# Performance work log

Measured on AMD Instinct MI355X. Metric: run time of the kernel, lower is better.

The kernel has to match this reference:

```python
import jax, jax.numpy as jnp
import numpy as np

D_MODEL = 1024
N_HEADS = 16
HEAD_DIM = D_MODEL // N_HEADS
D_FF = 4096
B, S = 2, 2048


def layer_norm(x, gamma, beta, eps=1e-5):
    mu = jnp.mean(x, axis=-1, keepdims=True)
    var = jnp.mean(jnp.square(x - mu), axis=-1, keepdims=True)
    return (x - mu) * jax.lax.rsqrt(var + eps) * gamma + beta


def setup_inputs() -> dict:
    key = jax.random.key(0)
    ks = jax.random.split(key, 8)
    s = 0.02
    return {
        "x": jax.random.normal(ks[0], (B, S, D_MODEL), dtype=jnp.float32),
        "qkv_w": jax.random.normal(ks[1], (D_MODEL, 3 * D_MODEL), dtype=jnp.float32) * s,
        "qkv_b": jnp.zeros((3 * D_MODEL,), jnp.float32),
        "out_w": jax.random.normal(ks[2], (D_MODEL, D_MODEL), dtype=jnp.float32) * s,
        "out_b": jnp.zeros((D_MODEL,), jnp.float32),
        "attn_ln_g": jnp.ones((D_MODEL,), jnp.float32),
        "attn_ln_b": jnp.zeros((D_MODEL,), jnp.float32),
        "norm1_g": jnp.ones((D_MODEL,), jnp.float32),
        "norm1_b": jnp.zeros((D_MODEL,), jnp.float32),
        "ff_ln_g": jnp.ones((D_MODEL,), jnp.float32),
        "ff_ln_b": jnp.zeros((D_MODEL,), jnp.float32),
        "w1": jax.random.normal(ks[3], (D_MODEL, D_FF), dtype=jnp.float32) * s,
        "b1": jnp.zeros((D_FF,), jnp.float32),
        "w2": jax.random.normal(ks[4], (D_FF, D_MODEL), dtype=jnp.float32) * s,
        "b2": jnp.zeros((D_MODEL,), jnp.float32),
        "norm2_g": jnp.ones((D_MODEL,), jnp.float32),
        "norm2_b": jnp.zeros((D_MODEL,), jnp.float32),
    }


def reference(x, qkv_w, qkv_b, out_w, out_b, attn_ln_g, attn_ln_b,
              norm1_g, norm1_b, ff_ln_g, ff_ln_b, w1, b1, w2, b2,
              norm2_g, norm2_b):
    # --- MultiHeadAttention (pre-LN inside the attn block) ---
    h = layer_norm(x, attn_ln_g, attn_ln_b)
    qkv = h @ qkv_w + qkv_b                       # [B,S,3D]
    qkv = qkv.reshape(B, S, 3, N_HEADS, HEAD_DIM)
    q = jnp.transpose(qkv[:, :, 0], (0, 2, 1, 3))  # [B,H,S,hd]
    k = jnp.transpose(qkv[:, :, 1], (0, 2, 1, 3))
    v = jnp.transpose(qkv[:, :, 2], (0, 2, 1, 3))
    scale = HEAD_DIM ** -0.5
    scores = jnp.einsum("bhqd,bhkd->bhqk", q, k) * scale  # [B,H,S,S]
    attn = jax.nn.softmax(scores, axis=-1)
    ctx = jnp.einsum("bhqk,bhkd->bhqd", attn, v)
    ctx = jnp.transpose(ctx, (0, 2, 1, 3)).reshape(B, S, D_MODEL)
    attn_out = ctx @ out_w + out_b

    # residual + post-LN
    x = layer_norm(x + attn_out, norm1_g, norm1_b)

    # --- FeedForward (pre-LN inside the FF block, GELU) ---
    h = layer_norm(x, ff_ln_g, ff_ln_b)
    ff = jax.nn.gelu(h @ w1 + b1, approximate=False) @ w2 + b2

    # residual + post-LN
    return layer_norm(x + ff, norm2_g, norm2_b)
```

## Files before the change

kernel.cpp:

```cpp
#include <hip/hip_runtime.h>
#include <hip/hip_bf16.h>

typedef __attribute__((ext_vector_type(4))) float f32x4;
typedef __attribute__((ext_vector_type(16))) float f32x16;
typedef __attribute__((ext_vector_type(8))) short s16x8;
typedef __attribute__((ext_vector_type(4))) short s16x4;

#define DM 1024
#define NH 16
#define NB 2
#define NS 2048
#define NTOK (NB*NS)

__device__ __forceinline__ float b2f(short u){
  union { unsigned int i; float f; } c; c.i = ((unsigned int)(unsigned short)u) << 16; return c.f;
}
__device__ __forceinline__ short f2b(float f){
  __hip_bfloat16 h = __float2bfloat16(f);
  return __builtin_bit_cast(short, h);
}
__device__ __forceinline__ unsigned pk2(float lo, float hi){
  unsigned ul = __builtin_bit_cast(unsigned, lo);
  unsigned uh = __builtin_bit_cast(unsigned, hi);
  return (uh & 0xFFFF0000u) | (ul >> 16);
}
__device__ __forceinline__ float ex2(float x){
  float r;
  asm("v_exp_f32 %0, %1" : "=v"(r) : "v"(x));
  return r;
}
__device__ __forceinline__ float rcpf(float x){
  float r;
  asm("v_rcp_f32 %0, %1" : "=v"(r) : "v"(x));
  return r;
}
__device__ __forceinline__ void gload16(const void* g, void* l){
  __builtin_amdgcn_global_load_lds((const __attribute__((address_space(1))) void*)g,
                                   (__attribute__((address_space(3))) void*)l, 16, 0, 0);
}
__device__ __forceinline__ s16x4 tr16(const void* p){
  s16x4 r;
  asm volatile("ds_read_b64_tr_b16 %0, %1"
               : "=v"(r)
               : "v"((const __attribute__((address_space(3))) short*)p)
               : "memory");
  return r;
}

#define BARX { __builtin_amdgcn_sched_barrier(0); __builtin_amdgcn_s_barrier(); __builtin_amdgcn_sched_barrier(0); }
#define LGK  { asm volatile("s_waitcnt lgkmcnt(0)" ::: "memory"); __builtin_amdgcn_sched_barrier(0); }

template<int MIH>
__device__ __forceinline__ void rdA(s16x8 (&Af)[4][2], const short* Ab, int foff){
  #pragma unroll
  for (int m=0;m<4;m++)
    #pragma unroll
    for (int ks=0;ks<2;ks++)
      Af[m][ks] = *(const s16x8*)(Ab + (MIH*4+m)*1024 + ks*512 + foff);
}
template<int NIH>
__device__ __forceinline__ void rdB(s16x8 (&Bf)[4][2], const short* Bb, int foff){
  #pragma unroll
  for (int n=0;n<2;n++)
    #pragma unroll
    for (int ks=0;ks<2;ks++)
      Bf[NIH*2+n][ks] = *(const s16x8*)(Bb + (NIH*2+n)*1024 + ks*512 + foff);
}
template<int MIH,int NIH>
__device__ __forceinline__ void mmQ(f32x4 (&acc)[8][4], s16x8 (&Af)[4][2], s16x8 (&Bf)[4][2]){
  __builtin_amdgcn_s_setprio(1);
  #pragma unroll
  for (int m=0;m<4;m++)
    #pragma unroll
    for (int n=0;n<2;n++)
      #pragma unroll
      for (int ks=0;ks<2;ks++)
        acc[MIH*4+m][NIH*2+n] = __builtin_amdgcn_mfma_f32_16x16x32_bf16(
            Af[m][ks], Bf[NIH*2+n][ks], acc[MIH*4+m][NIH*2+n], 0,0,0);
  __builtin_amdgcn_s_setprio(0);
}

template<int GELU, int SPLITS>
__global__ __launch_bounds__(512,2) void gemm8p(
    const short* __restrict__ A, const short* __restrict__ Bt,
    const float* __restrict__ bias,
    short* __restrict__ C0, short* __restrict__ C1,
    short* __restrict__ C2, short* __restrict__ C3,
    int M, int N, int Ktot)
{
  __shared__ short Al[2*16384];
  __shared__ short Bl[2*16384];
  int tid = threadIdx.x, wid = tid>>6, lane = tid&63;
  int la = lane&15, lb = lane>>4;
  int z = blockIdx.z;
  const int Ksp = Ktot / SPLITS;
  short* C = (SPLITS==1) ? C0 : (z==0?C0 : z==1?C1 : z==2?C2 : C3);
  const short* Az  = A  + z*Ksp;
  const short* Btz = Bt + z*Ksp;
  int nbn = N>>8;
  int nwg = (M>>8)*nbn;
  int bid = (int)blockIdx.x;
  int sid = (bid&7)*(nwg>>3) + (bid>>3);
  int bm = sid / nbn, bn = sid % nbn;
  int wm2 = wid>>2, wn4 = wid&3;
  int bhalf = wn4>>1, bq4 = (wn4&1)*4;

  const short* aA0 = Az  + (size_t)(bm*256)*Ktot;
  const short* aA1 = Az  + (size_t)(bm*256+128)*Ktot;
  const short* bB0 = Btz + (size_t)(bn*256)*Ktot;
  const short* bB1 = Btz + (size_t)(bn*256+128)*Ktot;

  auto stG = [&](short* dstHalf, const short* srcRow0, int kt){
    #pragma unroll
    for (int c=0;c<2;c++){
      int s = c*8 + wid;
      int row = ((s>>1)<<4) + (lane>>2);
      int kk  = kt + ((s&1)<<5) + (((lane&3)<<3) ^ ((lane&32)>>1));
      gload16(srcRow0 + (size_t)row*Ktot + kk, dstHalf + s*512);
    }
  };

  int NJ = Ksp>>7;
  stG(&Al[0], aA0, 0);      stG(&Al[8192], aA1, 0);
  stG(&Bl[0], bB0, 0);      stG(&Bl[8192], bB1, 0);
  stG(&Bl[16384], bB0, 64); stG(&Bl[16384+8192], bB1, 64);
  asm volatile("s_waitcnt vmcnt(4)" ::: "memory");
  BARX;

  f32x4 acc[8][4] = {};
  s16x8 Af[4][2], Bf[4][2];
  int foff = la*32 + ((lb*8) ^ ((la&8)<<1));

  const short* Ab0c = &Al[wm2*8192];
  const short* Ab1c = &Al[16384 + wm2*8192];
  const short* Bb0c = &Bl[bhalf*8192 + bq4*1024];
  const short* Bb1c = &Bl[16384 + bhalf*8192 + bq4*1024];

  for (int j=0;j<NJ;j++){
    bool more = (j+1 < NJ);
    int ktA  = (2*j+1)*64;
    int ktN0 = (2*j+2)*64, ktN1 = (2*j+3)*64;
    rdA<0>(Af, Ab0c, foff); rdB<0>(Bf, Bb0c, foff);
    stG(&Al[16384], aA0, ktA);
    BARX; LGK; mmQ<0,0>(acc,Af,Bf); BARX;
    rdB<1>(Bf, Bb0c, foff);
    stG(&Al[16384+8192], aA1, ktA);
    BARX; LGK; mmQ<0,1>(acc,Af,Bf); BARX;
    rdA<1>(Af, Ab0c, foff);
    if (more) stG(&Bl[0], bB0, ktN0);
    BARX; LGK; mmQ<1,1>(acc,Af,Bf); BARX;
    if (more){ stG(&Bl[8192], bB1, ktN0);
               asm volatile("s_waitcnt vmcnt(4)" ::: "memory"); }
    else     { asm volatile("s_waitcnt vmcnt(0)" ::: "memory"); }
    BARX; mmQ<1,0>(acc,Af,Bf); BARX;
    rdA<0>(Af, Ab1c, foff); rdB<0>(Bf, Bb1c, foff);
    if (more) stG(&Al[0], aA0, ktN0);
    BARX; LGK; mmQ<0,0>(acc,Af,Bf); BARX;
    rdB<1>(Bf, Bb1c, foff);
    if (more) stG(&Al[8192], aA1, ktN0);
    BARX; LGK; mmQ<0,1>(acc,Af,Bf); BARX;
    rdA<1>(Af, Ab1c, foff);
    if (more) stG(&Bl[16384], bB0, ktN1);
    BARX; LGK; mmQ<1,1>(acc,Af,Bf); BARX;
    if (more){ stG(&Bl[16384+8192], bB1, ktN1);
               asm volatile("s_waitcnt vmcnt(4)" ::: "memory"); }
    else     { asm volatile("s_waitcnt vmcnt(0)" ::: "memory"); }
    BARX; mmQ<1,0>(acc,Af,Bf); BARX;
  }

  short* halfC = wm2 ? Bl : Al;
  #pragma unroll
  for (int ni=0;ni<4;ni++){
    int col = wn4*64 + ni*16 + la;
    float bv = (SPLITS==1 || z==0) ? bias[bn*256 + col] : 0.0f;
    #pragma unroll
    for (int mi=0;mi<8;mi++){
      int rloc = mi*16 + lb*4;
      #pragma unroll
      for (int j=0;j<4;j++){
        float v = acc[mi][ni][j] + bv;
        if (GELU){
          float xx = v;
          float y = xx*(0.79788456f + 0.035677408f*xx*xx);
          float p = ex2(2.88539008f*y);
          v = xx - xx*rcpf(p + 1.0f);
        }
        halfC[(rloc+j)*256 + col] = f2b(v);
      }
    }
  }
  BARX;
  #pragma unroll
  for (int i=0;i<8;i++){
    int row = i*32 + (tid>>4);
    int colc = (tid&15)*16;
    const short* src = (i<4) ? &Al[(row&127)*256 + colc] : &Bl[(row&127)*256 + colc];
    s16x8 v0 = *(const s16x8*)src;
    s16x8 v1 = *(const s16x8*)(src+8);
    short* dst = &C[(size_t)(bm*256+row)*N + bn*256 + colc];
    *(s16x8*)dst = v0;
    *(s16x8*)(dst+8) = v1;
  }
}

__global__ __launch_bounds__(512,1) void attn_fwd(const short* __restrict__ qkv, short* __restrict__ ctx)
{
  __shared__ short KlS[2*4096];
  __shared__ short VlS[2*4096];
  __shared__ float stats[8*32];
  char* Kl = (char*)KlS; char* Vl = (char*)VlS;
  int tid=threadIdx.x, w=tid>>6, lane=tid&63;
  int q5=lane&31, hi=lane>>5, la=lane&15, lb0=(lane>>4)&1;
  int qt=blockIdx.x, bh=blockIdx.y;
  int b=bh>>4, h=bh&15;
  int q0w = qt*256 + w*32;

  const float QSC = 0.125f * 1.44269504f;
  const short* qp = qkv + (size_t)(b*NS+q0w+q5)*3072 + h*64 + hi*8;
  s16x8 qf[4];
  #pragma unroll
  for (int ds=0; ds<4; ds++){
    s16x8 v = *(const s16x8*)(qp + ds*16);
    #pragma unroll
    for (int j=0;j<8;j++) v[j] = f2b(b2f(v[j])*QSC);
    qf[ds]=v;
  }

  int krow = 8*w + (lane>>3);
  int kcolS = (((lane&7) ^ ((lane>>3)&7)) << 3);
  const short* Ksrc = qkv + (size_t)(b*NS+krow)*3072 + h*64 + 1024 + kcolS;
  int vk = 16*(w&3) + 8*hi + 4*lb0 + ((lane>>1)&3);
  int vd = 32*(w>>2) + 16*((lane>>3)&1) + 8*(lane&1);
  const short* Vsrc = qkv + (size_t)(b*NS+vk)*3072 + h*64 + 2048 + vd;

  int sw = (q5&7)<<4;
  int baseK = q5*128 + ((hi<<4) ^ (sw&16)) + (sw&96);
  int baseV = hi*512 + lb0*128 + la*8;

  f32x16 cacc0={}, cacc1={};
  float mrow=-1e30f, lrow=0.f;
  const size_t tstep = (size_t)64*3072;

  gload16(Ksrc, Kl + w*1024);
  gload16(Vsrc, Vl + w*1024);
  __syncthreads();
  int cur=0;

  for (int t=0;t<NS/64;t++){
    if (t+1 < NS/64){
      gload16(Ksrc + (size_t)(t+1)*tstep, Kl + (cur^1)*8192 + w*1024);
      gload16(Vsrc + (size_t)(t+1)*tstep, Vl + (cur^1)*8192 + w*1024);
    }
    const char* Kb = Kl + cur*8192;
    f32x16 s0={}, s1={};
    #pragma unroll
    for (int ds=0; ds<4; ds++){
      s16x8 k0 = *(const s16x8*)(Kb + (baseK ^ (ds<<5)));
      s16x8 k1 = *(const s16x8*)(Kb + 4096 + (baseK ^ (ds<<5)));
      s0 = __builtin_amdgcn_mfma_f32_32x32x16_bf16(k0, qf[ds], s0, 0,0,0);
      s1 = __builtin_amdgcn_mfma_f32_32x32x16_bf16(k1, qf[ds], s1, 0,0,0);
    }
    float pmax = s0[0];
    #pragma unroll
    for (int r=1;r<16;r++) pmax = fmaxf(pmax, s0[r]);
    #pragma unroll
    for (int r=0;r<16;r++) pmax = fmaxf(pmax, s1[r]);
    pmax = fmaxf(pmax, __shfl_xor(pmax, 32, 64));
    if (__any(pmax > mrow + 8.f)){
      float mnew = fmaxf(mrow, pmax);
      float corr = ex2(mrow - mnew);
      if (!hi) stats[w*32+q5] = corr;
      LGK;
      lrow *= corr; mrow = mnew;
      #pragma unroll
      for (int r=0;r<16;r++){
        float c = stats[w*32 + ((r&3)+8*(r>>2)+4*hi)];
        cacc0[r]*=c; cacc1[r]*=c;
      }
    }
    float rs = 0.f;
    #pragma unroll
    for (int r=0;r<16;r++){ float p=ex2(s0[r]-mrow); s0[r]=p; rs+=p; }
    #pragma unroll
    for (int r=0;r<16;r++){ float p=ex2(s1[r]-mrow); s1[r]=p; rs+=p; }
    rs += __shfl_xor(rs, 32, 64);
    lrow += rs;
    unsigned int D0[4][2], D1[4][2], R0[4][2], R1[4][2];
    #pragma unroll
    for (int bb=0;bb<4;bb++)
      #pragma unroll
      for (int hh=0;hh<2;hh++){
        D0[bb][hh] = pk2(s0[4*bb+2*hh], s0[4*bb+2*hh+1]);
        D1[bb][hh] = pk2(s1[4*bb+2*hh], s1[4*bb+2*hh+1]);
      }
    #pragma unroll
    for (int bb=0;bb<4;bb++)
      #pragma unroll
      for (int hh=0;hh<2;hh++){
        R0[bb][hh] = (unsigned int)__shfl_xor((int)D0[bb][hh], 32, 64);
        R1[bb][hh] = (unsigned int)__shfl_xor((int)D1[bb][hh], 32, 64);
      }
    union PA { unsigned int u[4]; s16x8 v; } pa[4];
    #pragma unroll
    for (int e=0;e<2;e++)
      #pragma unroll
      for (int hh=0;hh<2;hh++){
        pa[e].u[hh]     = hi ? R0[2*e+1][hh] : D0[2*e][hh];
        pa[e].u[2+hh]   = hi ? D0[2*e+1][hh] : R0[2*e][hh];
        pa[2+e].u[hh]   = hi ? R1[2*e+1][hh] : D1[2*e][hh];
        pa[2+e].u[2+hh] = hi ? D1[2*e+1][hh] : R1[2*e][hh];
      }
    const char* Vb = Vl + cur*8192;
    #pragma unroll
    for (int ks=0;ks<4;ks++){
      s16x4 t00 = tr16(Vb + ks*1024 +        0 + baseV);
      s16x4 t01 = tr16(Vb + ks*1024 +      256 + baseV);
      s16x4 t10 = tr16(Vb + ks*1024 + 4096     + baseV);
      s16x4 t11 = tr16(Vb + ks*1024 + 4096+256 + baseV);
      LGK;
      union { s16x4 hh[2]; s16x8 v; } u0, u1;
      u0.hh[0]=t00; u0.hh[1]=t01;
      u1.hh[0]=t10; u1.hh[1]=t11;
      cacc0 = __builtin_amdgcn_mfma_f32_32x32x16_bf16(pa[ks].v, u0.v, cacc0, 0,0,0);
      cacc1 = __builtin_amdgcn_mfma_f32_32x32x16_bf16(pa[ks].v, u1.v, cacc1, 0,0,0);
    }
    __syncthreads();
    cur ^= 1;
  }
  if (!hi) stats[w*32+q5] = 1.0f/lrow;
  LGK;
  #pragma unroll
  for (int r=0;r<16;r++){
    int q = (r&3)+8*(r>>2)+4*hi;
    float linv = stats[w*32+q];
    size_t row = (size_t)(b*NS + q0w + q)*DM + h*64;
    ctx[row + q5]      = f2b(cacc0[r]*linv);
    ctx[row + 32 + q5] = f2b(cacc1[r]*linv);
  }
}

__device__ __forceinline__ void wred2(float& s, float& ss){
  #pragma unroll
  for (int m=1;m<64;m<<=1){ s += __shfl_xor(s,m,64); ss += __shfl_xor(ss,m,64); }
}

__global__ __launch_bounds__(256) void ln_in(const float* __restrict__ x,
    const float* __restrict__ g, const float* __restrict__ be, short* __restrict__ out)
{
  int row=blockIdx.x, tid=threadIdx.x;
  __shared__ float r1[4], r2[4];
  float4 v = ((const float4*)(x + (size_t)row*DM))[tid];
  float s=v.x+v.y+v.z+v.w, ss=v.x*v.x+v.y*v.y+v.z*v.z+v.w*v.w;
  wred2(s,ss);
  if ((tid&63)==0){ r1[tid>>6]=s; r2[tid>>6]=ss; }
  __syncthreads();
  s=r1[0]+r1[1]+r1[2]+r1[3]; ss=r2[0]+r2[1]+r2[2]+r2[3];
  float mu=s*(1.f/DM);
  float rstd=rsqrtf(ss*(1.f/DM)-mu*mu+1e-5f);
  float4 gv=((const float4*)g)[tid], bv=((const float4*)be)[tid];
  s16x4 o;
  o[0]=f2b((v.x-mu)*rstd*gv.x+bv.x);
  o[1]=f2b((v.y-mu)*rstd*gv.y+bv.y);
  o[2]=f2b((v.z-mu)*rstd*gv.z+bv.z);
  o[3]=f2b((v.w-mu)*rstd*gv.w+bv.w);
  *(s16x4*)(out + (size_t)row*DM + tid*4) = o;
}

__global__ __launch_bounds__(256) void ln_chain(const float* __restrict__ x,
    const short* __restrict__ p0, const short* __restrict__ p1,
    const short* __restrict__ p2, const short* __restrict__ p3,
    const float* __restrict__ g1, const float* __restrict__ be1,
    const float* __restrict__ g2, const float* __restrict__ be2,
    float* __restrict__ x1, short* __restrict__ h2)
{
  int row=blockIdx.x, tid=threadIdx.x;
  __shared__ float r1[4], r2[4], r3[4], r4[4];
  size_t off = (size_t)row*DM + tid*4;
  float4 xv = ((const float4*)(x + (size_t)row*DM))[tid];
  s16x4 a0=*(const s16x4*)(p0+off), a1=*(const s16x4*)(p1+off);
  s16x4 a2=*(const s16x4*)(p2+off), a3=*(const s16x4*)(p3+off);
  float4 y;
  y.x = xv.x + b2f(a0[0])+b2f(a1[0])+b2f(a2[0])+b2f(a3[0]);
  y.y = xv.y + b2f(a0[1])+b2f(a1[1])+b2f(a2[1])+b2f(a3[1]);
  y.z = xv.z + b2f(a0[2])+b2f(a1[2])+b2f(a2[2])+b2f(a3[2]);
  y.w = xv.w + b2f(a0[3])+b2f(a1[3])+b2f(a2[3])+b2f(a3[3]);
  float s=y.x+y.y+y.z+y.w, ss=y.x*y.x+y.y*y.y+y.z*y.z+y.w*y.w;
  wred2(s,ss);
  if ((tid&63)==0){ r1[tid>>6]=s; r2[tid>>6]=ss; }
  __syncthreads();
  s=r1[0]+r1[1]+r1[2]+r1[3]; ss=r2[0]+r2[1]+r2[2]+r2[3];
  float mu=s*(1.f/DM);
  float rstd=rsqrtf(ss*(1.f/DM)-mu*mu+1e-5f);
  float4 g1v=((const float4*)g1)[tid], b1v=((const float4*)be1)[tid];
  float4 xo;
  xo.x=(y.x-mu)*rstd*g1v.x+b1v.x;
  xo.y=(y.y-mu)*rstd*g1v.y+b1v.y;
  xo.z=(y.z-mu)*rstd*g1v.z+b1v.z;
  xo.w=(y.w-mu)*rstd*g1v.w+b1v.w;
  ((float4*)(x1 + (size_t)row*DM))[tid] = xo;
  float s2=xo.x+xo.y+xo.z+xo.w, ss2=xo.x*xo.x+xo.y*xo.y+xo.z*xo.z+xo.w*xo.w;
  wred2(s2,ss2);
  if ((tid&63)==0){ r3[tid>>6]=s2; r4[tid>>6]=ss2; }
  __syncthreads();
  s2=r3[0]+r3[1]+r3[2]+r3[3]; ss2=r4[0]+r4[1]+r4[2]+r4[3];
  float mu2=s2*(1.f/DM);
  float rstd2=rsqrtf(ss2*(1.f/DM)-mu2*mu2+1e-5f);
  float4 g2v=((const float4*)g2)[tid], b2v=((const float4*)be2)[tid];
  s16x4 o;
  o[0]=f2b((xo.x-mu2)*rstd2*g2v.x+b2v.x);
  o[1]=f2b((xo.y-mu2)*rstd2*g2v.y+b2v.y);
  o[2]=f2b((xo.z-mu2)*rstd2*g2v.z+b2v.z);
  o[3]=f2b((xo.w-mu2)*rstd2*g2v.w+b2v.w);
  *(s16x4*)(h2 + off) = o;
}

__global__ __launch_bounds__(256) void ln_out_k(const float* __restrict__ x1,
    const short* __restrict__ p0, const short* __restrict__ p1,
    const short* __restrict__ p2, const short* __restrict__ p3,
    const float* __restrict__ g, const float* __restrict__ be, float* __restrict__ out)
{
  int row=blockIdx.x, tid=threadIdx.x;
  __shared__ float r1[4], r2[4];
  size_t off = (size_t)row*DM + tid*4;
  float4 xv = ((const float4*)(x1 + (size_t)row*DM))[tid];
  s16x4 a0=*(const s16x4*)(p0+off), a1=*(const s16x4*)(p1+off);
  s16x4 a2=*(const s16x4*)(p2+off), a3=*(const s16x4*)(p3+off);
  float4 y;
  y.x = xv.x + b2f(a0[0])+b2f(a1[0])+b2f(a2[0])+b2f(a3[0]);
  y.y = xv.y + b2f(a0[1])+b2f(a1[1])+b2f(a2[1])+b2f(a3[1]);
  y.z = xv.z + b2f(a0[2])+b2f(a1[2])+b2f(a2[2])+b2f(a3[2]);
  y.w = xv.w + b2f(a0[3])+b2f(a1[3])+b2f(a2[3])+b2f(a3[3]);
  float s=y.x+y.y+y.z+y.w, ss=y.x*y.x+y.y*y.y+y.z*y.z+y.w*y.w;
  wred2(s,ss);
  if ((tid&63)==0){ r1[tid>>6]=s; r2[tid>>6]=ss; }
  __syncthreads();
  s=r1[0]+r1[1]+r1[2]+r1[3]; ss=r2[0]+r2[1]+r2[2]+r2[3];
  float mu=s*(1.f/DM);
  float rstd=rsqrtf(ss*(1.f/DM)-mu*mu+1e-5f);
  float4 gv=((const float4*)g)[tid], bv=((const float4*)be)[tid];
  float4 o;
  o.x=(y.x-mu)*rstd*gv.x+bv.x;
  o.y=(y.y-mu)*rstd*gv.y+bv.y;
  o.z=(y.z-mu)*rstd*gv.z+bv.z;
  o.w=(y.w-mu)*rstd*gv.w+bv.w;
  ((float4*)(out + (size_t)row*DM))[tid] = o;
}

__global__ __launch_bounds__(256) void cast_t(const float* __restrict__ w, short* __restrict__ wt, int R, int C)
{
  __shared__ short t[64][65];
  int nbr = R>>6;
  int br = (int)blockIdx.x % nbr, bc = (int)blockIdx.x / nbr;
  int tid = threadIdx.x;
  #pragma unroll
  for (int i=0;i<4;i++){
    int c = i*256 + tid;
    int r = c>>4, c4 = (c&15)*4;
    float4 v = *(const float4*)(w + (size_t)(br*64 + r)*C + bc*64 + c4);
    t[r][c4+0]=f2b(v.x); t[r][c4+1]=f2b(v.y); t[r][c4+2]=f2b(v.z); t[r][c4+3]=f2b(v.w);
  }
  __syncthreads();
  #pragma unroll
  for (int i=0;i<4;i++){
    int c = i*256 + tid;
    int oc = c>>4, c4 = (c&15)*4;
    s16x4 p;
    p[0]=t[c4+0][oc]; p[1]=t[c4+1][oc]; p[2]=t[c4+2][oc]; p[3]=t[c4+3][oc];
    *(s16x4*)&wt[(size_t)(bc*64 + oc)*R + br*64 + c4] = p;
  }
}

extern "C" void kernel_launch(void* const* d_in, const int* in_sizes, int n_in,
                              void* d_out, int out_size, void* d_ws, size_t ws_size,
                              hipStream_t stream)
{
  const float* x      = (const float*)d_in[0];
  const float* qkv_w  = (const float*)d_in[1];
  const float* qkv_b  = (const float*)d_in[2];
  const float* out_w  = (const float*)d_in[3];
  const float* out_b  = (const float*)d_in[4];
  const float* aln_g  = (const float*)d_in[5];
  const float* aln_b  = (const float*)d_in[6];
  const float* n1_g   = (const float*)d_in[7];
  const float* n1_b   = (const float*)d_in[8];
  const float* fln_g  = (const float*)d_in[9];
  const float* fln_b  = (const float*)d_in[10];
  const float* w1     = (const float*)d_in[11];
  const float* b1     = (const float*)d_in[12];
  const float* w2     = (const float*)d_in[13];
  const float* b2     = (const float*)d_in[14];
  const float* n2_g   = (const float*)d_in[15];
  const float* n2_b   = (const float*)d_in[16];

  char* ws = (char*)d_ws;
  short* w2T   = (short*)(ws + 0);
  short* w1T   = (short*)(ws + 8388608);
  short* woutT = (short*)(ws + 16777216);
  short* wqkvT = (short*)(ws + 18874368);
  short* h1    = (short*)(ws + 25165824);
  short* qkv   = (short*)(ws + 33554432);
  short* ctx   = (short*)(ws + 58720256);
  float* x1    = (float*)(ws + 67108864);
  short* ff1   = (short*)(ws + 33554432);
  short* Po0 = (short*)(ws + 25165824);
  short* Po1 = (short*)(ws + 33554432);
  short* Po2 = (short*)(ws + 41943040);
  short* Po3 = (short*)(ws + 50331648);
  short* Pf0 = (short*)(ws + 8388608);
  short* Pf1 = (short*)(ws + 16777216);
  short* Pf2 = (short*)(ws + 25165824);
  short* Pf3 = (short*)(ws + 83886080);
  float* outp  = (float*)d_out;

  cast_t<<<dim3(16*48),256,0,stream>>>(qkv_w, wqkvT, 1024, 3072);
  cast_t<<<dim3(16*16),256,0,stream>>>(out_w, woutT, 1024, 1024);
  cast_t<<<dim3(16*64),256,0,stream>>>(w1,    w1T,   1024, 4096);
  cast_t<<<dim3(64*16),256,0,stream>>>(w2,    w2T,   4096, 1024);

  ln_in<<<NTOK,256,0,stream>>>(x, aln_g, aln_b, h1);
  gemm8p<0,1><<<dim3(192,1,1),512,0,stream>>>(h1, wqkvT, qkv_b, qkv,qkv,qkv,qkv, 4096,3072,1024);
  attn_fwd<<<dim3(8,32),512,0,stream>>>(qkv, ctx);
  gemm8p<0,4><<<dim3(64,1,4),512,0,stream>>>(ctx, woutT, out_b, Po0,Po1,Po2,Po3, 4096,1024,1024);
  ln_chain<<<NTOK,256,0,stream>>>(x, Po0,Po1,Po2,Po3, n1_g,n1_b, fln_g,fln_b, x1, h1);
  gemm8p<1,1><<<dim3(256,1,1),512,0,stream>>>(h1, w1T, b1, ff1,ff1,ff1,ff1, 4096,4096,1024);
  gemm8p<0,4><<<dim3(64,1,4),512,0,stream>>>(ff1, w2T, b2, Pf0,Pf1,Pf2,Pf3, 4096,1024,4096);
  ln_out_k<<<NTOK,256,0,stream>>>(x1, Pf0,Pf1,Pf2,Pf3, n2_g,n2_b, outp);
}
```

Before: 260.3 us.

## Split attention over the key dimension into two halves and merge partial results

Attention now runs split-K (flash-decoding style): each block handles half of the key sequence, grid z=2, and writes a normalized partial output plus per-row max and sum. A new merge kernel combines the two partials with log-sum-exp weights into ctx. This doubles the block count from 256 to 512 so the 256-CU GPU is filled better, and launch bounds allow 2 blocks per CU. The cost is an extra kernel launch, extra bf16 partial traffic, a second rounding to bf16, and workspace buffer reshuffling that must avoid aliasing.

```diff
diff --git a/kernel.cpp b/kernel.cpp
--- a/kernel.cpp
+++ b/kernel.cpp
@@ -203,7 +203,8 @@
   }
 }
 
-__global__ __launch_bounds__(512,1) void attn_fwd(const short* __restrict__ qkv, short* __restrict__ ctx)
+__global__ __launch_bounds__(512,2) void attn_fwd(const short* __restrict__ qkv,
+    short* __restrict__ Op0, short* __restrict__ Op1, float* __restrict__ ml)
 {
   __shared__ short KlS[2*4096];
   __shared__ short VlS[2*4096];
@@ -211,9 +212,12 @@
   char* Kl = (char*)KlS; char* Vl = (char*)VlS;
   int tid=threadIdx.x, w=tid>>6, lane=tid&63;
   int q5=lane&31, hi=lane>>5, la=lane&15, lb0=(lane>>4)&1;
-  int qt=blockIdx.x, bh=blockIdx.y;
+  int qt=blockIdx.x, bh=blockIdx.y, z=blockIdx.z;
   int b=bh>>4, h=bh&15;
   int q0w = qt*256 + w*32;
+  short* Od = z ? Op1 : Op0;
+  float* Md = ml + z*131072;
+  float* Ld = Md + 65536;
 
   const float QSC = 0.125f * 1.44269504f;
   const short* qp = qkv + (size_t)(b*NS+q0w+q5)*3072 + h*64 + hi*8;
@@ -226,12 +230,13 @@
     qf[ds]=v;
   }
 
+  const size_t tstep = (size_t)64*3072;
   int krow = 8*w + (lane>>3);
   int kcolS = (((lane&7) ^ ((lane>>3)&7)) << 3);
-  const short* Ksrc = qkv + (size_t)(b*NS+krow)*3072 + h*64 + 1024 + kcolS;
+  const short* Ksrc = qkv + (size_t)(b*NS+krow)*3072 + h*64 + 1024 + kcolS + (size_t)(z*16)*tstep;
   int vk = 16*(w&3) + 8*hi + 4*lb0 + ((lane>>1)&3);
   int vd = 32*(w>>2) + 16*((lane>>3)&1) + 8*(lane&1);
-  const short* Vsrc = qkv + (size_t)(b*NS+vk)*3072 + h*64 + 2048 + vd;
+  const short* Vsrc = qkv + (size_t)(b*NS+vk)*3072 + h*64 + 2048 + vd + (size_t)(z*16)*tstep;
 
   int sw = (q5&7)<<4;
   int baseK = q5*128 + ((hi<<4) ^ (sw&16)) + (sw&96);
@@ -239,15 +244,14 @@
 
   f32x16 cacc0={}, cacc1={};
   float mrow=-1e30f, lrow=0.f;
-  const size_t tstep = (size_t)64*3072;
 
   gload16(Ksrc, Kl + w*1024);
   gload16(Vsrc, Vl + w*1024);
   __syncthreads();
   int cur=0;
 
-  for (int t=0;t<NS/64;t++){
-    if (t+1 < NS/64){
+  for (int t=0;t<16;t++){
+    if (t+1 < 16){
       gload16(Ksrc + (size_t)(t+1)*tstep, Kl + (cur^1)*8192 + w*1024);
       gload16(Vsrc + (size_t)(t+1)*tstep, Vl + (cur^1)*8192 + w*1024);
     }
@@ -327,16 +331,43 @@
     __syncthreads();
     cur ^= 1;
   }
-  if (!hi) stats[w*32+q5] = 1.0f/lrow;
+  if (!hi){
+    stats[w*32+q5] = 1.0f/lrow;
+    Md[bh*2048 + q0w + q5] = mrow;
+    Ld[bh*2048 + q0w + q5] = lrow;
+  }
   LGK;
   #pragma unroll
   for (int r=0;r<16;r++){
     int q = (r&3)+8*(r>>2)+4*hi;
     float linv = stats[w*32+q];
     size_t row = (size_t)(b*NS + q0w + q)*DM + h*64;
-    ctx[row + q5]      = f2b(cacc0[r]*linv);
-    ctx[row + 32 + q5] = f2b(cacc1[r]*linv);
-  }
+    Od[row + q5]      = f2b(cacc0[r]*linv);
+    Od[row + 32 + q5] = f2b(cacc1[r]*linv);
+  }
+}
+
+__global__ __launch_bounds__(256) void attn_mrg(const short* __restrict__ O0,
+    const short* __restrict__ O1, const float* __restrict__ ml, short* __restrict__ ctx)
+{
+  int r = blockIdx.x, tid = threadIdx.x;
+  int b = r>>11, q = r&2047;
+  int c = tid*4;
+  int h = c>>6;
+  int idx = (b*16+h)*2048 + q;
+  float m0 = ml[idx],        l0 = ml[65536+idx];
+  float m1 = ml[131072+idx], l1 = ml[196608+idx];
+  float M = fmaxf(m0,m1);
+  float w0 = l0*ex2(m0-M), w1 = l1*ex2(m1-M);
+  float inv = rcpf(w0+w1);
+  w0 *= inv; w1 *= inv;
+  size_t off = (size_t)r*DM + c;
+  s16x4 a = *(const s16x4*)(O0+off);
+  s16x4 bb = *(const s16x4*)(O1+off);
+  s16x4 o;
+  #pragma unroll
+  for (int j=0;j<4;j++) o[j] = f2b(w0*b2f(a[j]) + w1*b2f(bb[j]));
+  *(s16x4*)(ctx+off) = o;
 }
 
 __device__ __forceinline__ void wred2(float& s, float& ss){
@@ -499,13 +530,16 @@
   short* wqkvT = (short*)(ws + 18874368);
   short* h1    = (short*)(ws + 25165824);
   short* qkv   = (short*)(ws + 33554432);
-  short* ctx   = (short*)(ws + 58720256);
   float* x1    = (float*)(ws + 67108864);
   short* ff1   = (short*)(ws + 33554432);
+  short* Op1   = (short*)(ws + 25165824);
+  short* Op0   = (short*)(ws + 58720256);
+  float* mlb   = (float*)(ws + 18874368);
+  short* ctx   = (short*)(ws + 33554432);
   short* Po0 = (short*)(ws + 25165824);
-  short* Po1 = (short*)(ws + 33554432);
-  short* Po2 = (short*)(ws + 41943040);
-  short* Po3 = (short*)(ws + 50331648);
+  short* Po1 = (short*)(ws + 41943040);
+  short* Po2 = (short*)(ws + 50331648);
+  short* Po3 = (short*)(ws + 58720256);
   short* Pf0 = (short*)(ws + 8388608);
   short* Pf1 = (short*)(ws + 16777216);
   short* Pf2 = (short*)(ws + 25165824);
@@ -519,7 +553,8 @@
 
   ln_in<<<NTOK,256,0,stream>>>(x, aln_g, aln_b, h1);
   gemm8p<0,1><<<dim3(192,1,1),512,0,stream>>>(h1, wqkvT, qkv_b, qkv,qkv,qkv,qkv, 4096,3072,1024);
-  attn_fwd<<<dim3(8,32),512,0,stream>>>(qkv, ctx);
+  attn_fwd<<<dim3(8,32,2),512,0,stream>>>(qkv, Op0, Op1, mlb);
+  attn_mrg<<<dim3(4096),256,0,stream>>>(Op0, Op1, mlb, ctx);
   gemm8p<0,4><<<dim3(64,1,4),512,0,stream>>>(ctx, woutT, out_b, Po0,Po1,Po2,Po3, 4096,1024,1024);
   ln_chain<<<NTOK,256,0,stream>>>(x, Po0,Po1,Po2,Po3, n1_g,n1_b, fln_g,fln_b, x1, h1);
   gemm8p<1,1><<<dim3(256,1,1),512,0,stream>>>(h1, w1T, b1, ff1,ff1,ff1,ff1, 4096,4096,1024);
```

Result: no change. 257.7 us (-1.0%).
